# Optimization experiments

Measured on AMD Instinct MI355X. Metric: run time of the kernel, lower is better.

The kernel has to match this reference:

```python
import jax, jax.numpy as jnp
import numpy as np

SQRT2 = 1.4142135623730951  # ScaleCostWeight(sqrt(2)) applied to residuals
N_ITERS = 10
DAMP = 1e-8  # tiny Tikhonov for numerical safety of the 6x6 solve


def _hat(phi):
    x, y, z = phi[0], phi[1], phi[2]
    o = jnp.zeros((), phi.dtype)
    return jnp.stack([jnp.stack([o, -z, y]),
                      jnp.stack([z, o, -x]),
                      jnp.stack([-y, x, o])])


def se3_exp(xi):
    # xi: [6] = [rho (trans), phi (rot)] -> 4x4 SE3 matrix
    rho, phi = xi[:3], xi[3:]
    theta2 = jnp.sum(phi * phi)
    small = theta2 < 1e-12
    theta2s = jnp.where(small, 1.0, theta2)  # double-where for safe grads
    theta = jnp.sqrt(theta2s)
    A = jnp.where(small, 1.0, jnp.sin(theta) / theta)
    B = jnp.where(small, 0.5, (1.0 - jnp.cos(theta)) / theta2s)
    C = jnp.where(small, 1.0 / 6.0, (theta - jnp.sin(theta)) / (theta2s * theta))
    K = _hat(phi)
    K2 = K @ K
    I3 = jnp.eye(3, dtype=xi.dtype)
    R = I3 + A * K + B * K2
    V = I3 + B * K + C * K2
    t = V @ rho
    top = jnp.concatenate([R, t[:, None]], axis=1)
    bot = jnp.array([[0.0, 0.0, 0.0, 1.0]], dtype=xi.dtype)
    return jnp.concatenate([top, bot], axis=0)


def se3_inv(T):
    R = T[..., :3, :3]
    t = T[..., :3, 3:]
    Rt = jnp.swapaxes(R, -1, -2)
    top = jnp.concatenate([Rt, -(Rt @ t)], axis=-1)
    bot = jnp.broadcast_to(jnp.array([0.0, 0.0, 0.0, 1.0], T.dtype),
                           T.shape[:-2] + (1, 4))
    return jnp.concatenate([top, bot], axis=-2)


def _r_single(xi, T, src3, trg3, Wh, w):
    # residual of one batch element at local perturbation xi (retract on right)
    Tn = T @ se3_exp(xi)
    pred = Tn[:3, :3] @ src3 + Tn[:3, 3:4]          # [3, N]
    e = trg3 - pred                                  # [3, N]
    ew = jnp.einsum('nij,jn->in', Wh, e) * w         # cholesky-weighted, w: [1,N]
    return (ew * SQRT2).reshape(-1)                  # [3N]


def _forward(src4, trg4, w, T_init, inv_cov, T_s_v):
    src3 = src4[:, :3, :]
    trg3 = trg4[:, :3, :]
    # W_half = cholesky(inv_cov)^T, computed once (aux var, constant over iters)
    Wh = jnp.swapaxes(jnp.linalg.cholesky(inv_cov), -1, -2)  # [B, N, 3, 3]
    B = src4.shape[0]
    I6 = jnp.eye(6, dtype=src4.dtype)

    def step(T, _):
        xi0 = jnp.zeros((B, 6), T.dtype)
        J = jax.vmap(jax.jacfwd(_r_single), in_axes=(0, 0, 0, 0, 0, 0))(
            xi0, T, src3, trg3, Wh, w)               # [B, 3N, 6]
        r = jax.vmap(_r_single)(xi0, T, src3, trg3, Wh, w)  # [B, 3N]
        g = jnp.einsum('bri,br->bi', J, r)
        H = jnp.einsum('bri,brj->bij', J, J) + DAMP * I6
        dx = -jnp.linalg.solve(H, g[..., None])[..., 0]
        return T @ jax.vmap(se3_exp)(dx), None

    T, _ = jax.lax.scan(step, T_init, None, length=N_ITERS)
    T_sv = jnp.broadcast_to(T_s_v, (B, 4, 4))
    return se3_inv(T_sv) @ T @ T_sv


def setup_inputs() -> dict:
    key = jax.random.key(0)
    B, N = 256, 2048
    k1, k2, k3, k4, k5, k6 = jax.random.split(key, 6)
    src3 = 2.0 * jax.random.normal(k1, (B, 3, N), dtype=jnp.float32)
    # well-posed registration problem: trg = T_true * src + noise
    T_true = jax.vmap(se3_exp)(0.3 * jax.random.normal(k2, (B, 6), dtype=jnp.float32))
    trg3 = (jnp.einsum('bij,bjn->bin', T_true[:, :3, :3], src3)
            + T_true[:, :3, 3:4]
            + 0.01 * jax.random.normal(k3, (B, 3, N), dtype=jnp.float32))
    ones = jnp.ones((B, 1, N), dtype=jnp.float32)
    keypoints_3D_src = jnp.concatenate([src3, ones], axis=1)
    keypoints_3D_trg = jnp.concatenate([trg3, ones], axis=1)
    weights = jax.random.uniform(k4, (B, 1, N), dtype=jnp.float32,
                                 minval=0.1, maxval=1.0)
    A = 0.3 * jax.random.normal(k5, (B, N, 3, 3), dtype=jnp.float32)
    inv_cov_weights = A @ jnp.swapaxes(A, -1, -2) + jnp.eye(3, dtype=jnp.float32)
    T_trg_src_init = jax.vmap(se3_exp)(
        0.05 * jax.random.normal(k6, (B, 6), dtype=jnp.float32))
    T_s_v = se3_exp(jnp.array([0.1, -0.2, 0.3, 0.2, -0.1, 0.15], dtype=jnp.float32))
    return {"keypoints_3D_src": keypoints_3D_src,
            "keypoints_3D_trg": keypoints_3D_trg,
            "weights": weights,
            "T_trg_src_init": T_trg_src_init,
            "inv_cov_weights": inv_cov_weights,
            "T_s_v": T_s_v}


def reference(keypoints_3D_src, keypoints_3D_trg, weights, T_trg_src_init,
              inv_cov_weights, T_s_v):
    return _forward(keypoints_3D_src, keypoints_3D_trg, weights,
                    T_trg_src_init, inv_cov_weights, T_s_v)
```

## Files before the change

### kernel.cpp

```cpp
#include <hip/hip_runtime.h>
#include <math.h>

#define NPTS   2048
#define BDIM   512
#define PPT    (NPTS / BDIM)
#define NW     (BDIM / 64)
#define NMOM   72
#define NITERS 10
#define DAMPF  1e-8f

__launch_bounds__(BDIM, 1)
__global__ void lie_gn_fused(const float* __restrict__ src4,
                             const float* __restrict__ trg4,
                             const float* __restrict__ wts,
                             const float* __restrict__ Tinit,
                             const float* __restrict__ icov,
                             const float* __restrict__ Tsv,
                             float* __restrict__ out)
{
    const int b    = blockIdx.x;
    const int tid  = threadIdx.x;
    const int lane = tid & 63;
    const int wid  = tid >> 6;

    __shared__ float red[NW][NMOM];
    __shared__ float mom_s[NMOM];

    const float* srcb = src4 + (size_t)b * 4 * NPTS;
    const float* trgb = trg4 + (size_t)b * 4 * NPTS;
    const float* wb   = wts  + (size_t)b * NPTS;
    const float* cb   = icov + (size_t)b * NPTS * 9;

    float acc[NMOM];
    #pragma unroll
    for (int k = 0; k < NMOM; ++k) acc[k] = 0.0f;

    #pragma unroll
    for (int kk = 0; kk < PPT; ++kk) {
        int n = tid + kk * BDIM;
        float sx = srcb[n], sy = srcb[NPTS + n], sz = srcb[2 * NPTS + n];
        float gx = trgb[n], gy = trgb[NPTS + n], gz = trgb[2 * NPTS + n];
        float w  = wb[n];
        const float* cc = cb + (size_t)n * 9;
        float w2 = 2.0f * w * w;
        float W[6];
        W[0] = w2 * cc[0];
        W[1] = w2 * cc[3];
        W[2] = w2 * cc[6];
        W[3] = w2 * cc[4];
        W[4] = w2 * cc[7];
        W[5] = w2 * cc[8];

        float hx = W[0] * gx + W[1] * gy + W[2] * gz;
        float hy = W[1] * gx + W[3] * gy + W[4] * gz;
        float hz = W[2] * gx + W[4] * gy + W[5] * gz;

        float sv[3] = { sx, sy, sz };
        float hv[3] = { hx, hy, hz };
        float ss[6] = { sx*sx, sx*sy, sx*sz, sy*sy, sy*sz, sz*sz };

        #pragma unroll
        for (int ij = 0; ij < 6; ++ij) {
            acc[ij] += W[ij];
            #pragma unroll
            for (int c2 = 0; c2 < 3; ++c2) acc[6 + ij * 3 + c2] += W[ij] * sv[c2];
            #pragma unroll
            for (int cd = 0; cd < 6; ++cd) acc[24 + ij * 6 + cd] += W[ij] * ss[cd];
        }
        acc[60] += hx; acc[61] += hy; acc[62] += hz;
        #pragma unroll
        for (int c2 = 0; c2 < 3; ++c2)
            #pragma unroll
            for (int i = 0; i < 3; ++i) acc[63 + c2 * 3 + i] += sv[c2] * hv[i];
    }

    float v36[36];
    #pragma unroll
    for (int k = 0; k < 36; ++k) {
        float lo  = acc[k],  hi  = acc[k + 36];
        float lox = __shfl_xor(lo, 32, 64);
        float hix = __shfl_xor(hi, 32, 64);
        v36[k] = (lane & 32) ? (hi + hix) : (lo + lox);
    }
    float v18[18];
    #pragma unroll
    for (int k = 0; k < 18; ++k) {
        float lo  = v36[k],  hi  = v36[k + 18];
        float lox = __shfl_xor(lo, 16, 64);
        float hix = __shfl_xor(hi, 16, 64);
        v18[k] = (lane & 16) ? (hi + hix) : (lo + lox);
    }
    #pragma unroll
    for (int k = 0; k < 18; ++k) {
        float v = v18[k];
        v += __shfl_xor(v, 8, 64);
        v += __shfl_xor(v, 4, 64);
        v += __shfl_xor(v, 2, 64);
        v += __shfl_xor(v, 1, 64);
        v18[k] = v;
    }
    if ((lane & 15) == 0) {
        int q = lane >> 4;
        #pragma unroll
        for (int k = 0; k < 18; ++k) red[wid][q * 18 + k] = v18[k];
    }
    __syncthreads();

    if (tid < NMOM) {
        float s = 0.0f;
        #pragma unroll
        for (int wv = 0; wv < NW; ++wv) s += red[wv][tid];
        mom_s[tid] = s;
    }
    __syncthreads();

    if (tid >= 64) return;

    float m[NMOM];
    #pragma unroll
    for (int k = 0; k < NMOM; ++k) m[k] = mom_s[k];

    float Rm[3][3], tv[3];
    #pragma unroll
    for (int i = 0; i < 3; ++i) {
        #pragma unroll
        for (int j = 0; j < 3; ++j) Rm[i][j] = Tinit[b * 16 + i * 4 + j];
        tv[i] = Tinit[b * 16 + i * 4 + 3];
    }

    const int SY[3][3] = { {0,1,2}, {1,3,4}, {2,4,5} };

    for (int it = 0; it < NITERS; ++it) {
        float C1[6][3];
        #pragma unroll
        for (int ij = 0; ij < 6; ++ij) {
            float a0 = m[6 + ij * 3 + 0], a1 = m[6 + ij * 3 + 1], a2 = m[6 + ij * 3 + 2];
            #pragma unroll
            for (int a = 0; a < 3; ++a)
                C1[ij][a] = Rm[a][0] * a0 + Rm[a][1] * a1 + Rm[a][2] * a2;
        }
        float SM[3][3], SWp[3];
        #pragma unroll
        for (int i = 0; i < 3; ++i) {
            SM[i][0] = C1[SY[i][1]][2] - C1[SY[i][2]][1];
            SM[i][1] = C1[SY[i][2]][0] - C1[SY[i][0]][2];
            SM[i][2] = C1[SY[i][0]][1] - C1[SY[i][1]][0];
            SWp[i]   = C1[SY[i][0]][0] + C1[SY[i][1]][1] + C1[SY[i][2]][2];
        }
        float P2[6][6];
        #pragma unroll
        for (int ij = 0; ij < 6; ++ij) {
            float S00 = m[24 + ij * 6 + 0], S01 = m[24 + ij * 6 + 1], S02 = m[24 + ij * 6 + 2];
            float S11 = m[24 + ij * 6 + 3], S12 = m[24 + ij * 6 + 4], S22 = m[24 + ij * 6 + 5];
            float U[3][3];
            #pragma unroll
            for (int a = 0; a < 3; ++a) {
                U[a][0] = Rm[a][0] * S00 + Rm[a][1] * S01 + Rm[a][2] * S02;
                U[a][1] = Rm[a][0] * S01 + Rm[a][1] * S11 + Rm[a][2] * S12;
                U[a][2] = Rm[a][0] * S02 + Rm[a][1] * S12 + Rm[a][2] * S22;
            }
            P2[0][ij] = U[0][0]*Rm[0][0] + U[0][1]*Rm[0][1] + U[0][2]*Rm[0][2];
            P2[1][ij] = U[0][0]*Rm[1][0] + U[0][1]*Rm[1][1] + U[0][2]*Rm[1][2];
            P2[2][ij] = U[0][0]*Rm[2][0] + U[0][1]*Rm[2][1] + U[0][2]*Rm[2][2];
            P2[3][ij] = U[1][0]*Rm[1][0] + U[1][1]*Rm[1][1] + U[1][2]*Rm[1][2];
            P2[4][ij] = U[1][0]*Rm[2][0] + U[1][1]*Rm[2][1] + U[1][2]*Rm[2][2];
            P2[5][ij] = U[2][0]*Rm[2][0] + U[2][1]*Rm[2][1] + U[2][2]*Rm[2][2];
        }
        float SN00 = -P2[5][3] + 2.f * P2[4][4] - P2[3][5];
        float SN01 = -P2[2][4] + P2[5][1] + P2[1][5] - P2[4][2];
        float SN02 = -P2[4][1] + P2[2][3] + P2[3][2] - P2[1][4];
        float SN11 =  2.f * P2[2][2] - P2[5][0] - P2[0][5];
        float SN12 =  P2[4][0] - P2[2][1] - P2[1][2] + P2[0][4];
        float SN22 = -P2[3][0] + 2.f * P2[1][1] - P2[0][3];

        float SWt0 = m[0]*tv[0] + m[1]*tv[1] + m[2]*tv[2];
        float SWt1 = m[1]*tv[0] + m[3]*tv[1] + m[4]*tv[2];
        float SWt2 = m[2]*tv[0] + m[4]*tv[1] + m[5]*tv[2];
        float Su[3] = { m[60] - SWp[0] - SWt0,
                        m[61] - SWp[1] - SWt1,
                        m[62] - SWp[2] - SWt2 };

        float G[3][3];
        #pragma unroll
        for (int a = 0; a < 3; ++a)
            #pragma unroll
            for (int bb = 0; bb < 3; ++bb)
                G[a][bb] = Rm[a][0]*m[63 + 0 + bb] + Rm[a][1]*m[63 + 3 + bb] + Rm[a][2]*m[63 + 6 + bb];
        float ch[3] = { G[1][2] - G[2][1], G[2][0] - G[0][2], G[0][1] - G[1][0] };
        float pw[3];
        pw[0] = P2[1][2] + P2[3][4] + P2[4][5] - P2[2][1] - P2[4][3] - P2[5][4];
        pw[1] = P2[2][0] + P2[4][1] + P2[5][2] - P2[0][2] - P2[1][4] - P2[2][5];
        pw[2] = P2[0][1] + P2[1][3] + P2[2][4] - P2[1][0] - P2[3][1] - P2[4][2];
        float Sq[3];
        #pragma unroll
        for (int i = 0; i < 3; ++i)
            Sq[i] = ch[i] - pw[i] + SM[0][i]*tv[0] + SM[1][i]*tv[1] + SM[2][i]*tv[2];

        float Hm[6][6];
        Hm[0][0] = m[0]; Hm[0][1] = m[1]; Hm[0][2] = m[2];
        Hm[1][1] = m[3]; Hm[1][2] = m[4]; Hm[2][2] = m[5];
        #pragma unroll
        for (int i = 0; i < 3; ++i) {
            Hm[i][3] = -SM[i][0]; Hm[i][4] = -SM[i][1]; Hm[i][5] = -SM[i][2];
        }
        Hm[3][3] = -SN00; Hm[3][4] = -SN01; Hm[3][5] = -SN02;
        Hm[4][4] = -SN11; Hm[4][5] = -SN12; Hm[5][5] = -SN22;
        #pragma unroll
        for (int i = 0; i < 6; ++i) {
            Hm[i][i] += DAMPF;
            #pragma unroll
            for (int j = 0; j < 6; ++j)
                if (j < i) Hm[i][j] = Hm[j][i];
        }
        float rhs[6] = { Su[0], Su[1], Su[2], Sq[0], Sq[1], Sq[2] };

        float L[6][6], dinv[6];
        #pragma unroll
        for (int i = 0; i < 6; ++i) {
            #pragma unroll
            for (int j = 0; j < 6; ++j) {
                if (j > i) continue;
                float sum = Hm[i][j];
                #pragma unroll
                for (int k2 = 0; k2 < 6; ++k2)
                    if (k2 < j) sum -= L[i][k2] * L[j][k2];
                if (i == j) { L[i][i] = sqrtf(sum); dinv[i] = 1.0f / L[i][i]; }
                else        L[i][j] = sum * dinv[j];
            }
        }
        float z[6];
        #pragma unroll
        for (int i = 0; i < 6; ++i) {
            float sum = rhs[i];
            #pragma unroll
            for (int k2 = 0; k2 < 6; ++k2)
                if (k2 < i) sum -= L[i][k2] * z[k2];
            z[i] = sum * dinv[i];
        }
        float y[6];
        #pragma unroll
        for (int i = 5; i >= 0; --i) {
            float sum = z[i];
            #pragma unroll
            for (int k2 = 0; k2 < 6; ++k2)
                if (k2 > i) sum -= L[k2][i] * y[k2];
            y[i] = sum * dinv[i];
        }

        float drx = Rm[0][0]*y[0] + Rm[1][0]*y[1] + Rm[2][0]*y[2];
        float dry = Rm[0][1]*y[0] + Rm[1][1]*y[1] + Rm[2][1]*y[2];
        float drz = Rm[0][2]*y[0] + Rm[1][2]*y[1] + Rm[2][2]*y[2];
        float dpx = Rm[0][0]*y[3] + Rm[1][0]*y[4] + Rm[2][0]*y[5];
        float dpy = Rm[0][1]*y[3] + Rm[1][1]*y[4] + Rm[2][1]*y[5];
        float dpz = Rm[0][2]*y[3] + Rm[1][2]*y[4] + Rm[2][2]*y[5];

        float th2  = dpx*dpx + dpy*dpy + dpz*dpz;
        bool  sm   = th2 < 1e-12f;
        float th2s = sm ? 1.0f : th2;
        float th   = sqrtf(th2s);
        float sth  = __sinf(th), cth = __cosf(th);
        float it2  = 1.0f / th2s;
        float Ae = sm ? 1.0f : sth / th;
        float Be = sm ? 0.5f : (1.0f - cth) * it2;
        float Ce = sm ? (1.0f / 6.0f) : (th - sth) * it2 / th;
        float Rd00 = 1.0f + Be * (dpx*dpx - th2);
        float Rd01 = -Ae * dpz + Be * dpx * dpy;
        float Rd02 =  Ae * dpy + Be * dpx * dpz;
        float Rd10 =  Ae * dpz + Be * dpx * dpy;
        float Rd11 = 1.0f + Be * (dpy*dpy - th2);
        float Rd12 = -Ae * dpx + Be * dpy * dpz;
        float Rd20 = -Ae * dpy + Be * dpx * dpz;
        float Rd21 =  Ae * dpx + Be * dpy * dpz;
        float Rd22 = 1.0f + Be * (dpz*dpz - th2);
        float V00 = 1.0f + Ce * (dpx*dpx - th2);
        float V01 = -Be * dpz + Ce * dpx * dpy;
        float V02 =  Be * dpy + Ce * dpx * dpz;
        float V10 =  Be * dpz + Ce * dpx * dpy;
        float V11 = 1.0f + Ce * (dpy*dpy - th2);
        float V12 = -Be * dpx + Ce * dpy * dpz;
        float V20 = -Be * dpy + Ce * dpx * dpz;
        float V21 =  Be * dpx + Ce * dpy * dpz;
        float V22 = 1.0f + Ce * (dpz*dpz - th2);
        float tdx = V00 * drx + V01 * dry + V02 * drz;
        float tdy = V10 * drx + V11 * dry + V12 * drz;
        float tdz = V20 * drx + V21 * dry + V22 * drz;

        float nR[3][3];
        nR[0][0] = Rm[0][0]*Rd00 + Rm[0][1]*Rd10 + Rm[0][2]*Rd20;
        nR[0][1] = Rm[0][0]*Rd01 + Rm[0][1]*Rd11 + Rm[0][2]*Rd21;
        nR[0][2] = Rm[0][0]*Rd02 + Rm[0][1]*Rd12 + Rm[0][2]*Rd22;
        nR[1][0] = Rm[1][0]*Rd00 + Rm[1][1]*Rd10 + Rm[1][2]*Rd20;
        nR[1][1] = Rm[1][0]*Rd01 + Rm[1][1]*Rd11 + Rm[1][2]*Rd21;
        nR[1][2] = Rm[1][0]*Rd02 + Rm[1][1]*Rd12 + Rm[1][2]*Rd22;
        nR[2][0] = Rm[2][0]*Rd00 + Rm[2][1]*Rd10 + Rm[2][2]*Rd20;
        nR[2][1] = Rm[2][0]*Rd01 + Rm[2][1]*Rd11 + Rm[2][2]*Rd21;
        nR[2][2] = Rm[2][0]*Rd02 + Rm[2][1]*Rd12 + Rm[2][2]*Rd22;
        float ntx = Rm[0][0]*tdx + Rm[0][1]*tdy + Rm[0][2]*tdz + tv[0];
        float nty = Rm[1][0]*tdx + Rm[1][1]*tdy + Rm[1][2]*tdz + tv[1];
        float ntz = Rm[2][0]*tdx + Rm[2][1]*tdy + Rm[2][2]*tdz + tv[2];
        #pragma unroll
        for (int i = 0; i < 3; ++i)
            #pragma unroll
            for (int j = 0; j < 3; ++j) Rm[i][j] = nR[i][j];
        tv[0] = ntx; tv[1] = nty; tv[2] = ntz;
    }

    if (lane == 0) {
        float R00 = Rm[0][0], R01 = Rm[0][1], R02 = Rm[0][2];
        float R10 = Rm[1][0], R11 = Rm[1][1], R12 = Rm[1][2];
        float R20 = Rm[2][0], R21 = Rm[2][1], R22 = Rm[2][2];
        float tx = tv[0], ty = tv[1], tz = tv[2];

        float Rv00 = Tsv[0], Rv01 = Tsv[1], Rv02 = Tsv[2],  tvx = Tsv[3];
        float Rv10 = Tsv[4], Rv11 = Tsv[5], Rv12 = Tsv[6],  tvy = Tsv[7];
        float Rv20 = Tsv[8], Rv21 = Tsv[9], Rv22 = Tsv[10], tvz = Tsv[11];

        float P00 = R00*Rv00 + R01*Rv10 + R02*Rv20;
        float P01 = R00*Rv01 + R01*Rv11 + R02*Rv21;
        float P02 = R00*Rv02 + R01*Rv12 + R02*Rv22;
        float P10 = R10*Rv00 + R11*Rv10 + R12*Rv20;
        float P11 = R10*Rv01 + R11*Rv11 + R12*Rv21;
        float P12 = R10*Rv02 + R11*Rv12 + R12*Rv22;
        float P20 = R20*Rv00 + R21*Rv10 + R22*Rv20;
        float P21 = R20*Rv01 + R21*Rv11 + R22*Rv21;
        float P22 = R20*Rv02 + R21*Rv12 + R22*Rv22;
        float Ptx = R00*tvx + R01*tvy + R02*tvz + tx;
        float Pty = R10*tvx + R11*tvy + R12*tvz + ty;
        float Ptz = R20*tvx + R21*tvy + R22*tvz + tz;

        float ex = Ptx - tvx, ey = Pty - tvy, ez = Ptz - tvz;
        float* o = out + (size_t)b * 16;
        o[0]  = Rv00*P00 + Rv10*P10 + Rv20*P20;
        o[1]  = Rv00*P01 + Rv10*P11 + Rv20*P21;
        o[2]  = Rv00*P02 + Rv10*P12 + Rv20*P22;
        o[3]  = Rv00*ex  + Rv10*ey  + Rv20*ez;
        o[4]  = Rv01*P00 + Rv11*P10 + Rv21*P20;
        o[5]  = Rv01*P01 + Rv11*P11 + Rv21*P21;
        o[6]  = Rv01*P02 + Rv11*P12 + Rv21*P22;
        o[7]  = Rv01*ex  + Rv11*ey  + Rv21*ez;
        o[8]  = Rv02*P00 + Rv12*P10 + Rv22*P20;
        o[9]  = Rv02*P01 + Rv12*P11 + Rv22*P21;
        o[10] = Rv02*P02 + Rv12*P12 + Rv22*P22;
        o[11] = Rv02*ex  + Rv12*ey  + Rv22*ez;
        o[12] = 0.0f; o[13] = 0.0f; o[14] = 0.0f; o[15] = 1.0f;
    }
}

extern "C" void kernel_launch(void* const* d_in, const int* in_sizes, int n_in,
                              void* d_out, int out_size, void* d_ws, size_t ws_size,
                              hipStream_t stream)
{
    const float* src4  = (const float*)d_in[0];
    const float* trg4  = (const float*)d_in[1];
    const float* wts   = (const float*)d_in[2];
    const float* Tinit = (const float*)d_in[3];
    const float* icov  = (const float*)d_in[4];
    const float* Tsv   = (const float*)d_in[5];

    const int B = in_sizes[3] / 16;

    hipLaunchKernelGGL(lie_gn_fused, dim3(B), dim3(BDIM), 0, stream,
                       src4, trg4, wts, Tinit, icov, Tsv, (float*)d_out);
}
```

Baseline: 114.3 us.

## Coalesce covariance loads via LDS transpose and use fast sqrt/rcp intrinsics

Each thread previously read its own 9-float covariance with a stride of 9 floats. Those loads now happen as coalesced wave-wide reads, are staged through shared memory and transposed back to per-point layout. All point data is also loaded up front to expose memory-level parallelism. In the serial solve and exponential map, sqrtf and divisions are replaced with the hardware sqrt and rcp approximations, which lowers precision slightly.

```diff
diff --git a/kernel.cpp b/kernel.cpp
--- a/kernel.cpp
+++ b/kernel.cpp
@@ -8,6 +8,9 @@
 #define NMOM   72
 #define NITERS 10
 #define DAMPF  1e-8f
+
+__device__ __forceinline__ float fsqrt(float x) { return __builtin_amdgcn_sqrtf(x); }
+__device__ __forceinline__ float frcp (float x) { return __builtin_amdgcn_rcpf(x); }
 
 __launch_bounds__(BDIM, 1)
 __global__ void lie_gn_fused(const float* __restrict__ src4,
@@ -23,6 +26,7 @@
     const int lane = tid & 63;
     const int wid  = tid >> 6;
 
+    __shared__ float stage[NW][576];
     __shared__ float red[NW][NMOM];
     __shared__ float mom_s[NMOM];
 
@@ -31,33 +35,53 @@
     const float* wb   = wts  + (size_t)b * NPTS;
     const float* cb   = icov + (size_t)b * NPTS * 9;
 
+    float sx[PPT], sy[PPT], sz[PPT], gx[PPT], gy[PPT], gz[PPT], wv[PPT];
+    float cv[PPT][9];
+
+    #pragma unroll
+    for (int kk = 0; kk < PPT; ++kk) {
+        int n = kk * BDIM + tid;
+        sx[kk] = srcb[n];
+        sy[kk] = srcb[NPTS + n];
+        sz[kk] = srcb[2 * NPTS + n];
+        gx[kk] = trgb[n];
+        gy[kk] = trgb[NPTS + n];
+        gz[kk] = trgb[2 * NPTS + n];
+        wv[kk] = wb[n];
+        const float* rp = cb + (size_t)(kk * BDIM + wid * 64) * 9;
+        #pragma unroll
+        for (int j = 0; j < 9; ++j) cv[kk][j] = rp[j * 64 + lane];
+    }
+
     float acc[NMOM];
     #pragma unroll
     for (int k = 0; k < NMOM; ++k) acc[k] = 0.0f;
 
     #pragma unroll
     for (int kk = 0; kk < PPT; ++kk) {
-        int n = tid + kk * BDIM;
-        float sx = srcb[n], sy = srcb[NPTS + n], sz = srcb[2 * NPTS + n];
-        float gx = trgb[n], gy = trgb[NPTS + n], gz = trgb[2 * NPTS + n];
-        float w  = wb[n];
-        const float* cc = cb + (size_t)n * 9;
-        float w2 = 2.0f * w * w;
+        #pragma unroll
+        for (int j = 0; j < 9; ++j) stage[wid][j * 64 + lane] = cv[kk][j];
+        float c[9];
+        #pragma unroll
+        for (int i = 0; i < 9; ++i) c[i] = stage[wid][lane * 9 + i];
+
+        float w2 = 2.0f * wv[kk] * wv[kk];
         float W[6];
-        W[0] = w2 * cc[0];
-        W[1] = w2 * cc[3];
-        W[2] = w2 * cc[6];
-        W[3] = w2 * cc[4];
-        W[4] = w2 * cc[7];
-        W[5] = w2 * cc[8];
-
-        float hx = W[0] * gx + W[1] * gy + W[2] * gz;
-        float hy = W[1] * gx + W[3] * gy + W[4] * gz;
-        float hz = W[2] * gx + W[4] * gy + W[5] * gz;
-
-        float sv[3] = { sx, sy, sz };
+        W[0] = w2 * c[0];
+        W[1] = w2 * c[3];
+        W[2] = w2 * c[6];
+        W[3] = w2 * c[4];
+        W[4] = w2 * c[7];
+        W[5] = w2 * c[8];
+
+        float hx = W[0] * gx[kk] + W[1] * gy[kk] + W[2] * gz[kk];
+        float hy = W[1] * gx[kk] + W[3] * gy[kk] + W[4] * gz[kk];
+        float hz = W[2] * gx[kk] + W[4] * gy[kk] + W[5] * gz[kk];
+
+        float sv[3] = { sx[kk], sy[kk], sz[kk] };
         float hv[3] = { hx, hy, hz };
-        float ss[6] = { sx*sx, sx*sy, sx*sz, sy*sy, sy*sz, sz*sz };
+        float ss[6] = { sv[0]*sv[0], sv[0]*sv[1], sv[0]*sv[2],
+                        sv[1]*sv[1], sv[1]*sv[2], sv[2]*sv[2] };
 
         #pragma unroll
         for (int ij = 0; ij < 6; ++ij) {
@@ -109,7 +133,7 @@
     if (tid < NMOM) {
         float s = 0.0f;
         #pragma unroll
-        for (int wv = 0; wv < NW; ++wv) s += red[wv][tid];
+        for (int wvi = 0; wvi < NW; ++wvi) s += red[wvi][tid];
         mom_s[tid] = s;
     }
     __syncthreads();
@@ -224,7 +248,7 @@
                 #pragma unroll
                 for (int k2 = 0; k2 < 6; ++k2)
                     if (k2 < j) sum -= L[i][k2] * L[j][k2];
-                if (i == j) { L[i][i] = sqrtf(sum); dinv[i] = 1.0f / L[i][i]; }
+                if (i == j) { L[i][i] = fsqrt(sum); dinv[i] = frcp(L[i][i]); }
                 else        L[i][j] = sum * dinv[j];
             }
         }
@@ -257,12 +281,13 @@
         float th2  = dpx*dpx + dpy*dpy + dpz*dpz;
         bool  sm   = th2 < 1e-12f;
         float th2s = sm ? 1.0f : th2;
-        float th   = sqrtf(th2s);
+        float th   = fsqrt(th2s);
+        float rth  = frcp(th);
         float sth  = __sinf(th), cth = __cosf(th);
-        float it2  = 1.0f / th2s;
-        float Ae = sm ? 1.0f : sth / th;
+        float it2  = frcp(th2s);
+        float Ae = sm ? 1.0f : sth * rth;
         float Be = sm ? 0.5f : (1.0f - cth) * it2;
-        float Ce = sm ? (1.0f / 6.0f) : (th - sth) * it2 / th;
+        float Ce = sm ? (1.0f / 6.0f) : (th - sth) * it2 * rth;
         float Rd00 = 1.0f + Be * (dpx*dpx - th2);
         float Rd01 = -Ae * dpz + Be * dpx * dpy;
         float Rd02 =  Ae * dpy + Be * dpx * dpz;
```

After: 115.7 us. Within noise of the previous version (+1.2%).
